# Optimization experiments

Measured on AMD Instinct MI355X. Metric: run time of the kernel, lower is better.

The kernel has to match this reference:

```python
import jax, jax.numpy as jnp
import numpy as np

B, S, D, H = 4, 2048, 1024, 16
DK = D // H

def setup_inputs() -> dict:
    key = jax.random.key(0)
    k1, k2, k3 = jax.random.split(key, 3)
    x = jax.random.normal(k1, (B, S, D), dtype=jnp.float32)
    # kaiming-uniform-ish scale for (d_k, d_model) fan_in = d_model
    bound = 1.0 / np.sqrt(D)
    w_qkv = jax.random.uniform(k2, (3, H, DK, D), dtype=jnp.float32, minval=-bound, maxval=bound)
    w_o = jax.random.uniform(k3, (D, D), dtype=jnp.float32, minval=-bound, maxval=bound)
    return {"x": x, "w_qkv": w_qkv, "w_o": w_o}

def reference(x, w_qkv, w_o):
    seq_len = x.shape[-2]
    d_k = w_qkv.shape[-2]
    # qkv projection: (b s m),(qkv h k m) -> (qkv b h s k)
    qkv = jnp.einsum('bsm,qhkm->qbhsk', x, w_qkv)
    Q, K, V = qkv[0], qkv[1], qkv[2]
    scores = jnp.einsum('bhqk,bhsk->bhqs', Q, K) / jnp.sqrt(jnp.float32(d_k))
    causal = jnp.triu(jnp.ones((seq_len, seq_len), dtype=bool), k=1)
    scores = jnp.where(causal, -jnp.inf, scores)
    probs = jax.nn.softmax(scores, axis=-1)  # (b h s s)
    attn = jnp.einsum('bhqs,bhsk->bhqk', probs, V)
    # concat heads: (b h s k) -> (b s h*k)
    attn = jnp.transpose(attn, (0, 2, 1, 3)).reshape(x.shape[0], seq_len, -1)
    # out proj: y = attn @ w_o.T
    return jnp.einsum('bsd,md->bsm', attn, w_o)
```

## Files before the change

kernel.cpp:

```cpp
#include <hip/hip_runtime.h>
#include <stdint.h>
#include <stddef.h>

typedef unsigned short u16;
typedef float  f32x4  __attribute__((ext_vector_type(4)));
typedef short  s16x8  __attribute__((ext_vector_type(8)));
typedef short  s16x4  __attribute__((ext_vector_type(4)));
typedef __bf16 bf16x8 __attribute__((ext_vector_type(8)));
typedef __bf16 bf16x4 __attribute__((ext_vector_type(4)));
typedef u16    u16x4  __attribute__((ext_vector_type(4)));

#define DEV static __device__ __forceinline__

DEV u16 f2bf(float f){
  uint32_t u = __builtin_bit_cast(uint32_t, f);
  u += 0x7FFFu + ((u >> 16) & 1u);
  return (u16)(u >> 16);
}

DEV f32x4 mfma16(s16x8 a, s16x8 b, f32x4 c){
  return __builtin_amdgcn_mfma_f32_16x16x32_bf16(
      __builtin_bit_cast(bf16x8, a), __builtin_bit_cast(bf16x8, b), c, 0, 0, 0);
}

DEV f32x4 mfma16k(s16x4 a, s16x4 b, f32x4 c){
  return __builtin_amdgcn_mfma_f32_16x16x16bf16_1k(a, b, c, 0, 0, 0);
}

DEV float exp2_fast(float x){ return __builtin_exp2f(x); }

DEV void gl_lds16(const u16* g, u16* l){
  __builtin_amdgcn_global_load_lds(
      (__attribute__((address_space(1))) void*)(g),
      (__attribute__((address_space(3))) void*)(l), 16, 0, 0);
}

__global__ __launch_bounds__(256) void cvt_all(const float* __restrict__ x,
                                               const float* __restrict__ wqkv,
                                               const float* __restrict__ wo,
                                               u16* __restrict__ outb){
  const int N1 = 2097152;
  const int N2 = N1 + 786432;
  const int NT = N2 + 262144;
  const int stride = gridDim.x * blockDim.x;
  for (int i = blockIdx.x * blockDim.x + threadIdx.x; i < NT; i += stride){
    const float* src; int j;
    if (i < N1){ src = x; j = i; }
    else if (i < N2){ src = wqkv; j = i - N1; }
    else { src = wo; j = i - N2; }
    float4 v = *(const float4*)(src + (size_t)j * 4);
    u16x4 o = { f2bf(v.x), f2bf(v.y), f2bf(v.z), f2bf(v.w) };
    *(u16x4*)(outb + (size_t)i * 4) = o;
  }
}

template<bool SWAPOP>
DEV void gemm_core(const u16* __restrict__ A, const u16* __restrict__ Bw,
                   int K, int bm, int bn, u16* ldsA, u16* ldsB, f32x4 acc[4][4])
{
  const int lane = threadIdx.x & 63;
  const int wave = threadIdx.x >> 6;
  const int wm = (wave >> 1) * 64, wn = (wave & 1) * 64;
  const int l8 = (lane & 7) * 8;
  const int lr = lane >> 3;
  const int fr = lane & 15;
  const int k8 = (lane >> 4) * 8;

  #pragma unroll
  for (int m = 0; m < 4; m++)
    #pragma unroll
    for (int n = 0; n < 4; n++){ f32x4 z = {0.f,0.f,0.f,0.f}; acc[m][n] = z; }

  const int nkt = K >> 6;
  for (int kt = 0; kt < nkt; ++kt){
    const int kb = kt * 64;
    #pragma unroll
    for (int i = 0; i < 4; i++){
      const int c   = wave * 4 + i;
      const int row = c * 8 + lr;
      gl_lds16(A  + (size_t)(bm + row) * K + kb + l8, ldsA + c * 512);
      gl_lds16(Bw + (size_t)(bn + row) * K + kb + l8, ldsB + c * 512);
    }
    __syncthreads();
    #pragma unroll
    for (int kk = 0; kk < 2; ++kk){
      s16x8 af[4], bfr[4];
      #pragma unroll
      for (int m = 0; m < 4; m++) af[m]  = *(const s16x8*)(ldsA + (wm + m*16 + fr)*64 + kk*32 + k8);
      #pragma unroll
      for (int n = 0; n < 4; n++) bfr[n] = *(const s16x8*)(ldsB + (wn + n*16 + fr)*64 + kk*32 + k8);
      #pragma unroll
      for (int m = 0; m < 4; m++)
        #pragma unroll
        for (int n = 0; n < 4; n++)
          acc[m][n] = SWAPOP ? mfma16(bfr[n], af[m], acc[m][n])
                             : mfma16(af[m], bfr[n], acc[m][n]);
    }
    __syncthreads();
  }
}

__global__ __launch_bounds__(256, 3) void gemm_qkv(const u16* __restrict__ xb,
                                                   const u16* __restrict__ wb,
                                                   u16* __restrict__ Qd,
                                                   u16* __restrict__ Kd,
                                                   u16* __restrict__ Vtd)
{
  __shared__ __align__(16) u16 ldsA[128*64];
  __shared__ __align__(16) u16 ldsB[128*64];
  f32x4 acc[4][4];
  const int bm = blockIdx.x * 128, bn = blockIdx.y * 128;
  const int q = bn >> 10;

  const int lane = threadIdx.x & 63, wave = threadIdx.x >> 6;
  const int wm = (wave >> 1) * 64, wn = (wave & 1) * 64;
  const int fr = lane & 15, r4 = (lane >> 4) * 4;

  if (q < 2){
    gemm_core<true>(xb, wb, 1024, bm, bn, ldsA, ldsB, acc);
    #pragma unroll
    for (int m = 0; m < 4; m++){
      const int s  = bm + wm + m*16 + fr;
      const int b  = s >> 11;
      const int s0 = s & 2047;
      #pragma unroll
      for (int n = 0; n < 4; n++){
        const int ng0 = bn + wn + n*16 + r4;
        const int h   = (ng0 >> 6) & 15, kd0 = ng0 & 63;
        const size_t bh = (size_t)(b * 16 + h);
        if (q == 0){
          u16x4 v = { f2bf(acc[m][n][0] * 0.18033688011112042f),
                      f2bf(acc[m][n][1] * 0.18033688011112042f),
                      f2bf(acc[m][n][2] * 0.18033688011112042f),
                      f2bf(acc[m][n][3] * 0.18033688011112042f) };
          *(u16x4*)(Qd + (bh*2048 + s0)*64 + kd0) = v;
        } else {
          u16x4 v = { f2bf(acc[m][n][0]), f2bf(acc[m][n][1]),
                      f2bf(acc[m][n][2]), f2bf(acc[m][n][3]) };
          *(u16x4*)(Kd + (bh*2048 + s0)*64 + kd0) = v;
        }
      }
    }
  } else {
    gemm_core<false>(xb, wb, 1024, bm, bn, ldsA, ldsB, acc);
    #pragma unroll
    for (int m = 0; m < 4; m++){
      const int i0 = bm + wm + m*16 + r4;
      const int b  = i0 >> 11;
      const int s0 = i0 & 2047;
      #pragma unroll
      for (int n = 0; n < 4; n++){
        const int ng = bn + wn + n*16 + fr;
        const int h  = (ng >> 6) & 15, kd = ng & 63;
        const size_t bh = (size_t)(b * 16 + h);
        u16x4 v = { f2bf(acc[m][n][0]), f2bf(acc[m][n][1]),
                    f2bf(acc[m][n][2]), f2bf(acc[m][n][3]) };
        *(u16x4*)(Vtd + (bh*64 + kd)*2048 + s0) = v;
      }
    }
  }
}

__global__ __launch_bounds__(256, 3) void gemm_outp(const u16* __restrict__ attnb,
                                                    const u16* __restrict__ wob,
                                                    float* __restrict__ C)
{
  __shared__ __align__(16) u16 ldsA[128*64];
  __shared__ __align__(16) u16 ldsB[128*64];
  f32x4 acc[4][4];
  const int bm = blockIdx.x * 128, bn = blockIdx.y * 128;
  gemm_core<true>(attnb, wob, 1024, bm, bn, ldsA, ldsB, acc);

  const int lane = threadIdx.x & 63, wave = threadIdx.x >> 6;
  const int wm = (wave >> 1) * 64, wn = (wave & 1) * 64;
  const int fr = lane & 15, r4 = (lane >> 4) * 4;
  #pragma unroll
  for (int m = 0; m < 4; m++){
    const int i0 = bm + wm + m*16 + fr;
    #pragma unroll
    for (int n = 0; n < 4; n++){
      const int ng0 = bn + wn + n*16 + r4;
      *(f32x4*)(C + (size_t)i0 * 1024 + ng0) = acc[m][n];
    }
  }
}

DEV void softmax_pack(f32x4 (&sc)[4], s16x4 (&pb)[4], int kb, int q0,
                      int fr, int r4)
{
  if (kb + 63 > q0){
    const int q_g = q0 + fr;
    #pragma unroll
    for (int mi = 0; mi < 4; mi++)
      #pragma unroll
      for (int r = 0; r < 4; r++){
        const int s_g = kb + mi*16 + r4 + r;
        sc[mi][r] = (s_g > q_g) ? -1e30f : sc[mi][r];
      }
  }
  #pragma unroll
  for (int mi = 0; mi < 4; mi++){
    f32x4 e;
    #pragma unroll
    for (int r = 0; r < 4; r++)
      e[r] = exp2_fast(sc[mi][r]);
    pb[mi] = __builtin_bit_cast(s16x4, __builtin_convertvector(e, bf16x4));
  }
}

DEV void chunk_step1(const u16* Kc, const u16* Vc, int kb, int q0,
                     const s16x8 (&qf)[2], f32x4 (&O)[4], f32x4 &L,
                     s16x4 ones, int fr, int g, int f, int r4)
{
  f32x4 sc[4];
  #pragma unroll
  for (int mi = 0; mi < 4; mi++){ f32x4 z = {0.f,0.f,0.f,0.f}; sc[mi] = z; }
  __builtin_amdgcn_s_setprio(1);
  #pragma unroll
  for (int kk = 0; kk < 2; kk++)
    #pragma unroll
    for (int mi = 0; mi < 4; mi++){
      s16x8 kf = *(const s16x8*)(Kc + (mi*16 + fr)*64 + ((kk*4 + g) ^ f)*8);
      sc[mi] = mfma16(kf, qf[kk], sc[mi]);
    }
  __builtin_amdgcn_s_setprio(0);

  s16x4 pb[4];
  softmax_pack(sc, pb, kb, q0, fr, r4);

  __builtin_amdgcn_s_setprio(1);
  #pragma unroll
  for (int mi = 0; mi < 4; mi++){
    L = mfma16k(ones, pb[mi], L);
    #pragma unroll
    for (int n = 0; n < 4; n++){
      s16x4 vf = *(const s16x4*)(Vc + (n*16 + fr)*64 + ((2*mi + (g >> 1)) ^ f)*8 + (g & 1)*4);
      O[n] = mfma16k(vf, pb[mi], O[n]);
    }
  }
  __builtin_amdgcn_s_setprio(0);
}

DEV void chunk_step2(const u16* Kc, const u16* Vc, int kb, int qh0, int ql0,
                     const s16x8 (&qfh)[2], const s16x8 (&qfl)[2],
                     f32x4 (&Oh)[4], f32x4 (&Ol)[4], f32x4 &Lh, f32x4 &Ll,
                     s16x4 ones, int fr, int g, int f, int r4)
{
  f32x4 sch[4], scl[4];
  #pragma unroll
  for (int mi = 0; mi < 4; mi++){
    f32x4 z = {0.f,0.f,0.f,0.f}; sch[mi] = z; scl[mi] = z;
  }
  __builtin_amdgcn_s_setprio(1);
  #pragma unroll
  for (int kk = 0; kk < 2; kk++)
    #pragma unroll
    for (int mi = 0; mi < 4; mi++){
      s16x8 kf = *(const s16x8*)(Kc + (mi*16 + fr)*64 + ((kk*4 + g) ^ f)*8);
      sch[mi] = mfma16(kf, qfh[kk], sch[mi]);
      scl[mi] = mfma16(kf, qfl[kk], scl[mi]);
    }
  __builtin_amdgcn_s_setprio(0);

  s16x4 pbh[4], pbl[4];
  softmax_pack(sch, pbh, kb, qh0, fr, r4);
  softmax_pack(scl, pbl, kb, ql0, fr, r4);

  __builtin_amdgcn_s_setprio(1);
  #pragma unroll
  for (int mi = 0; mi < 4; mi++){
    Lh = mfma16k(ones, pbh[mi], Lh);
    Ll = mfma16k(ones, pbl[mi], Ll);
    #pragma unroll
    for (int n = 0; n < 4; n++){
      s16x4 vf = *(const s16x4*)(Vc + (n*16 + fr)*64 + ((2*mi + (g >> 1)) ^ f)*8 + (g & 1)*4);
      Oh[n] = mfma16k(vf, pbh[mi], Oh[n]);
      Ol[n] = mfma16k(vf, pbl[mi], Ol[n]);
    }
  }
  __builtin_amdgcn_s_setprio(0);
}

__global__ __launch_bounds__(256, 4) void attn_fwd(const u16* __restrict__ Qd,
                                                   const u16* __restrict__ Kd,
                                                   const u16* __restrict__ Vtd,
                                                   u16* __restrict__ attnb)
{
  __shared__ __align__(16) u16 Kl[2][64*64];
  __shared__ __align__(16) u16 Vl[2][64*64];

  const int t = threadIdx.x;
  const int lane = t & 63, w = t >> 6;
  const int wg = blockIdx.x;
  const int bh = 8 * (wg & 7) + (wg >> 7);
  const int ph = (wg >> 3) & 15;
  const int p  = ph >> 1, half = ph & 1;
  const int qh = 8 + p, ql = 7 - p;
  const u16* Qp = Qd  + (size_t)bh * 2048 * 64;
  const u16* Kp = Kd  + (size_t)bh * 2048 * 64;
  const u16* Vp = Vtd + (size_t)bh * 64 * 2048;

  const int fr = lane & 15, g = lane >> 4;
  const int f  = fr & 7;
  const int k8 = g * 8, r4 = g * 4;
  const int rgs = half * 4 + w;
  const int qh0 = qh * 128 + rgs * 16;
  const int ql0 = ql * 128 + rgs * 16;
  const int nkt = 2 * qh + 2;

  const s16x4 ones = { 0x3F80, 0x3F80, 0x3F80, 0x3F80 };

  s16x8 qfh[2], qfl[2];
  #pragma unroll
  for (int kk = 0; kk < 2; kk++){
    qfh[kk] = *(const s16x8*)(Qp + (size_t)(qh0 + fr) * 64 + kk*32 + k8);
    qfl[kk] = *(const s16x8*)(Qp + (size_t)(ql0 + fr) * 64 + kk*32 + k8);
  }

  f32x4 Ohi[4], Olo[4], Lhi, Llo;
  #pragma unroll
  for (int n = 0; n < 4; n++){
    f32x4 z = {0.f,0.f,0.f,0.f}; Ohi[n] = z; Olo[n] = z;
  }
  { f32x4 z = {0.f,0.f,0.f,0.f}; Lhi = z; Llo = z; }

  const int Lr  = t >> 3;
  const int cs8 = ((t & 7) ^ (Lr & 7)) * 8;
  const u16* kS = Kp + Lr * 64 + cs8;
  const u16* vS = Vp + (size_t)Lr * 2048 + cs8;

  gl_lds16(kS,         (u16*)Kl + t*8);
  gl_lds16(kS + 2048,  (u16*)Kl + t*8 + 2048);
  gl_lds16(vS,         (u16*)Vl + t*8);
  gl_lds16(vS + 65536, (u16*)Vl + t*8 + 2048);
  kS += 4096; vS += 64;

  for (int kt = 0; kt < nkt; ++kt){
    __syncthreads();
    const int cur = kt & 1;
    if (kt + 1 < nkt){
      u16* kD = (u16*)Kl + (cur ^ 1) * 4096 + t*8;
      u16* vD = (u16*)Vl + (cur ^ 1) * 4096 + t*8;
      gl_lds16(kS,         kD);
      gl_lds16(kS + 2048,  kD + 2048);
      gl_lds16(vS,         vD);
      gl_lds16(vS + 65536, vD + 2048);
    }
    kS += 4096; vS += 64;

    const int kb = kt * 64;
    const u16* Kc = Kl[cur];
    const u16* Vc = Vl[cur];

    if (kb <= ql0 + 15)
      chunk_step2(Kc, Vc, kb, qh0, ql0, qfh, qfl,
                  Ohi, Olo, Lhi, Llo, ones, fr, g, f, r4);
    else if (kb <= qh0 + 15)
      chunk_step1(Kc, Vc, kb, qh0, qfh, Ohi, Lhi, ones, fr, g, f, r4);
  }

  const int b = bh >> 4, h = bh & 15;
  const float invh = 1.0f / Lhi[0];
  const float invl = 1.0f / Llo[0];
  const int sh = qh0 + fr;
  const int sl = ql0 + fr;
  #pragma unroll
  for (int n = 0; n < 4; n++){
    u16x4 vh = { f2bf(Ohi[n][0]*invh), f2bf(Ohi[n][1]*invh),
                 f2bf(Ohi[n][2]*invh), f2bf(Ohi[n][3]*invh) };
    *(u16x4*)(attnb + (((size_t)b*2048 + sh)*16 + h)*64 + n*16 + r4) = vh;
    u16x4 vl = { f2bf(Olo[n][0]*invl), f2bf(Olo[n][1]*invl),
                 f2bf(Olo[n][2]*invl), f2bf(Olo[n][3]*invl) };
    *(u16x4*)(attnb + (((size_t)b*2048 + sl)*16 + h)*64 + n*16 + r4) = vl;
  }
}

extern "C" void kernel_launch(void* const* d_in, const int* in_sizes, int n_in,
                              void* d_out, int out_size, void* d_ws, size_t ws_size,
                              hipStream_t stream)
{
  const float* x    = (const float*)d_in[0];
  const float* wqkv = (const float*)d_in[1];
  const float* wo   = (const float*)d_in[2];
  float* out = (float*)d_out;

  char* ws = (char*)d_ws;
  u16* xb    = (u16*)(ws);
  u16* wqb   = (u16*)(ws + 16777216);
  u16* wob   = (u16*)(ws + 23068672);
  u16* Qd    = (u16*)(ws + 25165824);
  u16* Kd    = (u16*)(ws + 41943040);
  u16* Vtd   = (u16*)(ws + 58720256);
  u16* attnb = xb;

  cvt_all<<<3072, 256, 0, stream>>>(x, wqkv, wo, xb);
  gemm_qkv<<<dim3(64, 24), 256, 0, stream>>>(xb, wqb, Qd, Kd, Vtd);
  attn_fwd<<<dim3(1024), 256, 0, stream>>>(Qd, Kd, Vtd, attnb);
  gemm_outp<<<dim3(64, 8), 256, 0, stream>>>(attnb, wob, out);
}
```

Before: 217.3 us.

## Swizzle GEMM LDS layout and remap GEMM tiles for XCD-local reuse

The GEMM core now stores LDS rows with an XOR swizzle on 16-byte chunks and reads fragments with the matching swizzle, aiming to remove bank conflicts on the MFMA fragment loads. Both projection GEMMs switch to a 1D grid whose block index is remapped so that blocks landing on the same XCD share M-tiles, improving L2 reuse of the A operand. The attention kernel's occupancy hint changes from a launch-bounds minimum of 4 blocks to amdgpu_waves_per_eu(4,4), and a helper is renamed. This risks a changed register budget for the attention kernel and depends on round-robin XCD dispatch for the tile mapping to pay off.

Measured after the change: 219.3 us. No clear change (+0.9%).

```diff
diff --git a/kernel.cpp b/kernel.cpp
--- a/kernel.cpp
+++ b/kernel.cpp
@@ -61,10 +61,11 @@
   const int lane = threadIdx.x & 63;
   const int wave = threadIdx.x >> 6;
   const int wm = (wave >> 1) * 64, wn = (wave & 1) * 64;
-  const int l8 = (lane & 7) * 8;
   const int lr = lane >> 3;
+  const int l8 = (((lane & 7) ^ lr) << 3);
   const int fr = lane & 15;
-  const int k8 = (lane >> 4) * 8;
+  const int g  = lane >> 4;
+  const int f  = fr & 7;
 
   #pragma unroll
   for (int m = 0; m < 4; m++)
@@ -86,9 +87,11 @@
     for (int kk = 0; kk < 2; ++kk){
       s16x8 af[4], bfr[4];
       #pragma unroll
-      for (int m = 0; m < 4; m++) af[m]  = *(const s16x8*)(ldsA + (wm + m*16 + fr)*64 + kk*32 + k8);
-      #pragma unroll
-      for (int n = 0; n < 4; n++) bfr[n] = *(const s16x8*)(ldsB + (wn + n*16 + fr)*64 + kk*32 + k8);
+      for (int m = 0; m < 4; m++)
+        af[m]  = *(const s16x8*)(ldsA + (wm + m*16 + fr)*64 + (((kk*4 + g) ^ f) << 3));
+      #pragma unroll
+      for (int n = 0; n < 4; n++)
+        bfr[n] = *(const s16x8*)(ldsB + (wn + n*16 + fr)*64 + (((kk*4 + g) ^ f) << 3));
       #pragma unroll
       for (int m = 0; m < 4; m++)
         #pragma unroll
@@ -109,8 +112,12 @@
   __shared__ __align__(16) u16 ldsA[128*64];
   __shared__ __align__(16) u16 ldsB[128*64];
   f32x4 acc[4][4];
-  const int bm = blockIdx.x * 128, bn = blockIdx.y * 128;
-  const int q = bn >> 10;
+  const int wg  = blockIdx.x;
+  const int xcd = wg & 7, rr = wg >> 3;
+  const int bm  = (xcd * 8 + (rr & 7)) * 128;
+  const int bnt = rr >> 3;
+  const int bn  = bnt * 128;
+  const int q   = bnt >> 3;
 
   const int lane = threadIdx.x & 63, wave = threadIdx.x >> 6;
   const int wm = (wave >> 1) * 64, wn = (wave & 1) * 64;
@@ -168,7 +175,10 @@
   __shared__ __align__(16) u16 ldsA[128*64];
   __shared__ __align__(16) u16 ldsB[128*64];
   f32x4 acc[4][4];
-  const int bm = blockIdx.x * 128, bn = blockIdx.y * 128;
+  const int wg  = blockIdx.x;
+  const int xcd = wg & 7, rr = wg >> 3;
+  const int bm  = (xcd * 8 + (rr & 7)) * 128;
+  const int bn  = (rr >> 3) * 128;
   gemm_core<true>(attnb, wob, 1024, bm, bn, ldsA, ldsB, acc);
 
   const int lane = threadIdx.x & 63, wave = threadIdx.x >> 6;
@@ -241,10 +251,10 @@
   __builtin_amdgcn_s_setprio(0);
 }
 
-DEV void chunk_step2(const u16* Kc, const u16* Vc, int kb, int qh0, int ql0,
-                     const s16x8 (&qfh)[2], const s16x8 (&qfl)[2],
-                     f32x4 (&Oh)[4], f32x4 (&Ol)[4], f32x4 &Lh, f32x4 &Ll,
-                     s16x4 ones, int fr, int g, int f, int r4)
+DEV void chunk_dual(const u16* Kc, const u16* Vc, int kb, int qh0, int ql0,
+                    const s16x8 (&qfh)[2], const s16x8 (&qfl)[2],
+                    f32x4 (&Oh)[4], f32x4 (&Ol)[4], f32x4 &Lh, f32x4 &Ll,
+                    s16x4 ones, int fr, int g, int f, int r4)
 {
   f32x4 sch[4], scl[4];
   #pragma unroll
@@ -281,10 +291,11 @@
   __builtin_amdgcn_s_setprio(0);
 }
 
-__global__ __launch_bounds__(256, 4) void attn_fwd(const u16* __restrict__ Qd,
-                                                   const u16* __restrict__ Kd,
-                                                   const u16* __restrict__ Vtd,
-                                                   u16* __restrict__ attnb)
+__attribute__((amdgpu_waves_per_eu(4, 4)))
+__global__ __launch_bounds__(256) void attn_fwd(const u16* __restrict__ Qd,
+                                                const u16* __restrict__ Kd,
+                                                const u16* __restrict__ Vtd,
+                                                u16* __restrict__ attnb)
 {
   __shared__ __align__(16) u16 Kl[2][64*64];
   __shared__ __align__(16) u16 Vl[2][64*64];
@@ -353,8 +364,8 @@
     const u16* Vc = Vl[cur];
 
     if (kb <= ql0 + 15)
-      chunk_step2(Kc, Vc, kb, qh0, ql0, qfh, qfl,
-                  Ohi, Olo, Lhi, Llo, ones, fr, g, f, r4);
+      chunk_dual(Kc, Vc, kb, qh0, ql0, qfh, qfl,
+                 Ohi, Olo, Lhi, Llo, ones, fr, g, f, r4);
     else if (kb <= qh0 + 15)
       chunk_step1(Kc, Vc, kb, qh0, qfh, Ohi, Lhi, ones, fr, g, f, r4);
   }
@@ -394,7 +405,7 @@
   u16* attnb = xb;
 
   cvt_all<<<3072, 256, 0, stream>>>(x, wqkv, wo, xb);
-  gemm_qkv<<<dim3(64, 24), 256, 0, stream>>>(xb, wqb, Qd, Kd, Vtd);
+  gemm_qkv<<<dim3(1536), 256, 0, stream>>>(xb, wqb, Qd, Kd, Vtd);
   attn_fwd<<<dim3(1024), 256, 0, stream>>>(Qd, Kd, Vtd, attnb);
-  gemm_outp<<<dim3(64, 8), 256, 0, stream>>>(attnb, wob, out);
-}
+  gemm_outp<<<dim3(512), 256, 0, stream>>>(attnb, wob, out);
+}
```
